# Performance work log

Measured on AMD Instinct MI355X. Metric: run time of the kernel, lower is better.

## Reference

```python
import jax, jax.numpy as jnp
from jax import lax
import numpy as np

S, B, XD = 2048, 64, 64   # seq_len, batch, x_dim
DX = 128                   # dense_x[-1]
H = 256                    # dim_RNN
DH = 128                   # dense_h_x[-1]
ALPHAS = np.array([0.9, 0.5, 0.1, 0.01], dtype=np.float32)


def setup_inputs() -> dict:
    key = jax.random.key(0)
    ks = jax.random.split(key, 12)
    def lin(k, fan_in, shape):
        return jax.random.normal(k, shape, jnp.float32) / np.sqrt(fan_in)
    sigmas = jnp.asarray(-np.log(1.0 / ALPHAS - 1.0), jnp.float32)  # inverse sigmoid
    return {
        "x": jax.random.normal(ks[0], (S, B, XD), jnp.float32),
        "Wx": lin(ks[1], XD, (XD, DX)),   # feature_extractor_x linear
        "bx": jnp.zeros((DX,), jnp.float32),
        "Wih": lin(ks[2], DX, (H, DX)),   # RNN input-hidden
        "bih": jnp.zeros((H,), jnp.float32),
        "Whh": lin(ks[3], H, (H, H)),     # RNN hidden-hidden
        "bhh": jnp.zeros((H,), jnp.float32),
        "Whx": lin(ks[4], H, (H, DH)),    # mlp_h_x linear
        "bhx": jnp.zeros((DH,), jnp.float32),
        "Wout": lin(ks[5], DH, (DH, XD)), # gen_out
        "bout": jnp.zeros((XD,), jnp.float32),
        "sigmas": sigmas,
    }


def reference(x, Wx, bx, Wih, bih, Whh, bhh, Whx, bhx, Wout, bout, sigmas):
    # alphas_per_unit: sigmoid(sigmas) tiled to dim_RNN
    alphas = jnp.tile(jax.nn.sigmoid(sigmas), H // sigmas.shape[0])  # [H]
    # feature extractor over all timesteps (teacher forcing, mix_ratio=0)
    feat = jnp.tanh(x @ Wx + bx)  # [S, B, DX]
    h0 = jnp.zeros((x.shape[1], H), x.dtype)

    def step(h, f_t):
        # emit y_t from previous hidden state: gen_out(tanh(mlp_h_x(h)))
        y_t = jnp.tanh(h @ Whx + bhx) @ Wout + bout        # [B, XD]
        # single-step Elman RNN cell
        h_new = jnp.tanh(f_t @ Wih.T + bih + h @ Whh.T + bhh)
        # leaky integration blend per unit
        h_next = (1.0 - alphas) * h + alphas * h_new
        return h_next, y_t

    _, y = lax.scan(step, h0, feat)  # y: [S, B, XD]
    return y
```

## Files before the change

kernel.cpp:

```cpp
#include <hip/hip_runtime.h>
#include <math.h>

#define SS 2048
#define BB 64
#define XDIM 64
#define DXF 128
#define HH 256
#define DHH 128

typedef float v2f __attribute__((ext_vector_type(2)));

__device__ __forceinline__ float ftanh(float x) {
    float e = __expf(2.0f * x);
    return 1.0f - 2.0f / (e + 1.0f);
}

template <int CTRL>
__device__ __forceinline__ float dpp_mov_f(float x) {
    return __int_as_float(__builtin_amdgcn_update_dpp(
        0, __float_as_int(x), CTRL, 0xF, 0xF, true));
}
#define RED8_SHR(s) { s += dpp_mov_f<0x111>(s); s += dpp_mov_f<0x112>(s); \
                      s += dpp_mov_f<0x114>(s); }
#define RED8_SHL(s) { s += dpp_mov_f<0x101>(s); s += dpp_mov_f<0x102>(s); \
                      s += dpp_mov_f<0x104>(s); }

__global__ __launch_bounds__(256) void k1_featu(
    const float* __restrict__ x, const float* __restrict__ Wx,
    const float* __restrict__ bx, const float* __restrict__ Wih,
    const float* __restrict__ bih, const float* __restrict__ bhh,
    float* __restrict__ u)
{
    __shared__ float xs[64][XDIM];
    __shared__ float fs[64][DXF];
    const int tid = threadIdx.x;
    const size_t row0 = (size_t)blockIdx.x * 64;

    for (int v = tid; v < 64 * XDIM; v += 256) {
        int r = v >> 6, m = v & 63;
        xs[r][m] = x[(row0 + r) * XDIM + m];
    }
    __syncthreads();

    {
        const int cq = tid & 31;
        const int ru = tid >> 5;
        v2f aA[2][4], aB[2][4];
        #pragma unroll
        for (int g = 0; g < 2; ++g)
            #pragma unroll
            for (int i = 0; i < 4; ++i) { aA[g][i] = (v2f)0.f; aB[g][i] = (v2f)0.f; }

        #pragma unroll
        for (int kc = 0; kc < 4; ++kc) {
            v2f wA[16], wB[16];
            #pragma unroll
            for (int k = 0; k < 16; ++k) {
                const float* wp = Wx + (kc * 16 + k) * DXF + cq;
                wA[k] = (v2f){wp[0],  wp[32]};
                wB[k] = (v2f){wp[64], wp[96]};
            }
            #pragma unroll
            for (int g = 0; g < 2; ++g) {
                const int rb = 8 * ru + 4 * g;
                #pragma unroll
                for (int k4 = 0; k4 < 4; ++k4) {
                    float4 xv[4];
                    #pragma unroll
                    for (int i = 0; i < 4; ++i)
                        xv[i] = *(const float4*)&xs[rb + i][kc * 16 + 4 * k4];
                    #pragma unroll
                    for (int i = 0; i < 4; ++i) {
                        #pragma unroll
                        for (int e = 0; e < 4; ++e) {
                            const float xe = (e == 0) ? xv[i].x : (e == 1) ? xv[i].y
                                           : (e == 2) ? xv[i].z : xv[i].w;
                            const v2f xb = (v2f){xe, xe};
                            aA[g][i] += wA[4 * k4 + e] * xb;
                            aB[g][i] += wB[4 * k4 + e] * xb;
                        }
                    }
                }
            }
        }
        const float b0 = bx[cq], b1 = bx[cq + 32], b2 = bx[cq + 64], b3 = bx[cq + 96];
        #pragma unroll
        for (int g = 0; g < 2; ++g)
            #pragma unroll
            for (int i = 0; i < 4; ++i) {
                const int r = 8 * ru + 4 * g + i;
                fs[r][cq]      = ftanh(aA[g][i].x + b0);
                fs[r][cq + 32] = ftanh(aA[g][i].y + b1);
                fs[r][cq + 64] = ftanh(aB[g][i].x + b2);
                fs[r][cq + 96] = ftanh(aB[g][i].y + b3);
            }
    }
    __syncthreads();

    {
        const int q4 = tid & 63;
        const int rq = tid >> 6;
        v2f aA[4][4], aB[4][4];
        #pragma unroll
        for (int g = 0; g < 4; ++g)
            #pragma unroll
            for (int i = 0; i < 4; ++i) { aA[g][i] = (v2f)0.f; aB[g][i] = (v2f)0.f; }

        #pragma unroll
        for (int kc = 0; kc < 8; ++kc) {
            v2f wA[16], wB[16];
            #pragma unroll
            for (int k4 = 0; k4 < 4; ++k4) {
                const float4 w0 = *(const float4*)(Wih + (size_t)(q4      ) * DXF + kc * 16 + 4 * k4);
                const float4 w1 = *(const float4*)(Wih + (size_t)(q4 +  64) * DXF + kc * 16 + 4 * k4);
                const float4 w2 = *(const float4*)(Wih + (size_t)(q4 + 128) * DXF + kc * 16 + 4 * k4);
                const float4 w3 = *(const float4*)(Wih + (size_t)(q4 + 192) * DXF + kc * 16 + 4 * k4);
                wA[4 * k4 + 0] = (v2f){w0.x, w1.x}; wA[4 * k4 + 1] = (v2f){w0.y, w1.y};
                wA[4 * k4 + 2] = (v2f){w0.z, w1.z}; wA[4 * k4 + 3] = (v2f){w0.w, w1.w};
                wB[4 * k4 + 0] = (v2f){w2.x, w3.x}; wB[4 * k4 + 1] = (v2f){w2.y, w3.y};
                wB[4 * k4 + 2] = (v2f){w2.z, w3.z}; wB[4 * k4 + 3] = (v2f){w2.w, w3.w};
            }
            #pragma unroll
            for (int g = 0; g < 4; ++g) {
                const int rb = 16 * rq + 4 * g;
                #pragma unroll
                for (int k4 = 0; k4 < 4; ++k4) {
                    float4 fv[4];
                    #pragma unroll
                    for (int i = 0; i < 4; ++i)
                        fv[i] = *(const float4*)&fs[rb + i][kc * 16 + 4 * k4];
                    #pragma unroll
                    for (int i = 0; i < 4; ++i) {
                        #pragma unroll
                        for (int e = 0; e < 4; ++e) {
                            const float fe = (e == 0) ? fv[i].x : (e == 1) ? fv[i].y
                                           : (e == 2) ? fv[i].z : fv[i].w;
                            const v2f fb = (v2f){fe, fe};
                            aA[g][i] += wA[4 * k4 + e] * fb;
                            aB[g][i] += wB[4 * k4 + e] * fb;
                        }
                    }
                }
            }
        }
        const float b0 = bih[q4]       + bhh[q4];
        const float b1 = bih[q4 + 64]  + bhh[q4 + 64];
        const float b2 = bih[q4 + 128] + bhh[q4 + 128];
        const float b3 = bih[q4 + 192] + bhh[q4 + 192];
        #pragma unroll
        for (int g = 0; g < 4; ++g)
            #pragma unroll
            for (int i = 0; i < 4; ++i) {
                const size_t row = row0 + 16 * rq + 4 * g + i;
                u[row * HH + q4]       = aA[g][i].x + b0;
                u[row * HH + q4 + 64]  = aA[g][i].y + b1;
                u[row * HH + q4 + 128] = aB[g][i].x + b2;
                u[row * HH + q4 + 192] = aB[g][i].y + b3;
            }
    }
}

__global__ __launch_bounds__(1024)
__attribute__((amdgpu_waves_per_eu(4, 4)))
void k2_rnn(
    const float* __restrict__ u, const float* __restrict__ Whh,
    const float* __restrict__ sigmas, float* __restrict__ hist)
{
    __shared__ float hbuf[2][HH];
    const int tid = threadIdx.x;
    const int b = blockIdx.x;
    const int c = tid & 7;
    const int rg = tid >> 3;

    v2f w2[2][16];
    #pragma unroll
    for (int r = 0; r < 2; ++r) {
        const float* wrow = Whh + (size_t)(2 * rg + r) * HH + 32 * c;
        #pragma unroll
        for (int j = 0; j < 8; ++j) {
            const int kk = 4 * ((j + c) & 7);
            const float4 wv = *(const float4*)(wrow + kk);
            w2[r][2 * j]     = (v2f){wv.x, wv.y};
            w2[r][2 * j + 1] = (v2f){wv.z, wv.w};
        }
    }

#define K2_PIN                                                               \
    _Pragma("unroll")                                                        \
    for (int r = 0; r < 2; ++r) {                                            \
        asm volatile("" : "+v"(w2[r][0]),  "+v"(w2[r][1]),  "+v"(w2[r][2]),  \
                          "+v"(w2[r][3]),  "+v"(w2[r][4]),  "+v"(w2[r][5]),  \
                          "+v"(w2[r][6]),  "+v"(w2[r][7]),  "+v"(w2[r][8]),  \
                          "+v"(w2[r][9]),  "+v"(w2[r][10]), "+v"(w2[r][11]), \
                          "+v"(w2[r][12]), "+v"(w2[r][13]), "+v"(w2[r][14]), \
                          "+v"(w2[r][15]));                                  \
    }
    K2_PIN

    const bool updHi = (c == 7);
    const bool updLo = (c == 0);
    const bool upd = updHi || updLo;
    const int myrow = 2 * rg + (updHi ? 0 : 1);

    const float alpha = 1.f / (1.f + __expf(-sigmas[myrow & 3]));

    if (tid < HH) hbuf[0][tid] = 0.0f;

    const size_t ustride = (size_t)BB * HH;
    const float* up = u + (size_t)b * HH + myrow;
    float uq0 = 0.f, uq1 = 0.f, uq2 = 0.f, uq3 = 0.f;
    if (upd) {
        uq0 = up[0];
        uq1 = up[ustride];
        uq2 = up[2 * ustride];
        uq3 = up[3 * ustride];
    }
    up += 4 * ustride;
    float* hp = hist + (size_t)b * HH + myrow;
    float hreg = 0.f;

    __syncthreads();

#define K2_BODY(T, UQ)                                                       \
    {                                                                        \
        const int cur = (T) & 1;                                             \
        float unew = 0.f;                                                    \
        if (upd && (T) + 4 < SS) unew = *up;     \
        up += ustride;                                                       \
        v2f a0a = (v2f)0.f, a0b = (v2f)0.f;                                  \
        v2f a1a = (v2f)0.f, a1b = (v2f)0.f;                                  \
        const float4* h4p = (const float4*)&hbuf[cur][32 * c];               \
        _Pragma("unroll")                                                    \
        for (int j = 0; j < 8; ++j) {                                        \
            const float4 h4 = h4p[(j + c) & 7];                              \
            const v2f hA = (v2f){h4.x, h4.y};                                \
            const v2f hB = (v2f){h4.z, h4.w};                                \
            a0a += w2[0][2 * j] * hA; a0b += w2[0][2 * j + 1] * hB;          \
            a1a += w2[1][2 * j] * hA; a1b += w2[1][2 * j + 1] * hB;          \
        }                                                                    \
        float s0 = (a0a.x + a0a.y) + (a0b.x + a0b.y);                        \
        float s1 = (a1a.x + a1a.y) + (a1b.x + a1b.y);                        \
        RED8_SHR(s0)                        \
        RED8_SHL(s1)                        \
        if (upd) {                                                           \
            const float s = (updHi ? s0 : s1) + (UQ);                        \
            *hp = hreg;                            \
            hreg = hreg + alpha * (ftanh(s) - hreg);                         \
            hbuf[cur ^ 1][myrow] = hreg;                                     \
            (UQ) = unew;                                                     \
        }                                                                    \
        hp += ustride;                                                       \
         \
        asm volatile("s_waitcnt lgkmcnt(0)\n\ts_barrier" ::: "memory");      \
    }

    for (int t = 0; t < SS; t += 4) {
        K2_PIN
        K2_BODY(t,     uq0)
        K2_BODY(t + 1, uq1)
        K2_BODY(t + 2, uq2)
        K2_BODY(t + 3, uq3)
    }
#undef K2_BODY
#undef K2_PIN
}

__global__ __launch_bounds__(256) void k3_y(
    const float* __restrict__ hist, const float* __restrict__ Whx,
    const float* __restrict__ bhx, const float* __restrict__ Wout,
    const float* __restrict__ bout, float* __restrict__ y)
{
    __shared__ float hs[32][HH];
    __shared__ float gs[32][DHH];
    const int tid = threadIdx.x;
    const size_t row0 = (size_t)blockIdx.x * 32;

    for (int v = tid; v < 32 * HH; v += 256) {
        int r = v >> 8, i = v & 255;
        hs[r][i] = hist[(row0 + r) * HH + i];
    }
    __syncthreads();

    {
        const int aq = tid & 31;
        const int ru = tid >> 5;
        v2f aA[4], aB[4];
        #pragma unroll
        for (int i = 0; i < 4; ++i) { aA[i] = (v2f)0.f; aB[i] = (v2f)0.f; }

        #pragma unroll
        for (int kc = 0; kc < 16; ++kc) {
            v2f wA[16], wB[16];
            #pragma unroll
            for (int k = 0; k < 16; ++k) {
                const float* wp = Whx + (size_t)(kc * 16 + k) * DHH + aq;
                wA[k] = (v2f){wp[0],  wp[32]};
                wB[k] = (v2f){wp[64], wp[96]};
            }
            #pragma unroll
            for (int k4 = 0; k4 < 4; ++k4) {
                float4 hv[4];
                #pragma unroll
                for (int i = 0; i < 4; ++i)
                    hv[i] = *(const float4*)&hs[4 * ru + i][kc * 16 + 4 * k4];
                #pragma unroll
                for (int i = 0; i < 4; ++i) {
                    #pragma unroll
                    for (int e = 0; e < 4; ++e) {
                        const float he = (e == 0) ? hv[i].x : (e == 1) ? hv[i].y
                                       : (e == 2) ? hv[i].z : hv[i].w;
                        const v2f hb = (v2f){he, he};
                        aA[i] += wA[4 * k4 + e] * hb;
                        aB[i] += wB[4 * k4 + e] * hb;
                    }
                }
            }
        }
        const float b0 = bhx[aq], b1 = bhx[aq + 32], b2 = bhx[aq + 64], b3 = bhx[aq + 96];
        #pragma unroll
        for (int i = 0; i < 4; ++i) {
            const int r = 4 * ru + i;
            gs[r][aq]      = ftanh(aA[i].x + b0);
            gs[r][aq + 32] = ftanh(aA[i].y + b1);
            gs[r][aq + 64] = ftanh(aB[i].x + b2);
            gs[r][aq + 96] = ftanh(aB[i].y + b3);
        }
    }
    __syncthreads();

    {
        const int o2 = tid & 31;
        const int ru = tid >> 5;
        v2f acc[4];
        #pragma unroll
        for (int i = 0; i < 4; ++i) acc[i] = (v2f)0.f;

        #pragma unroll
        for (int kc = 0; kc < 2; ++kc) {
            v2f w[64];
            #pragma unroll
            for (int k = 0; k < 64; ++k) {
                const float* wp = Wout + (size_t)(kc * 64 + k) * XDIM + o2;
                w[k] = (v2f){wp[0], wp[32]};
            }
            #pragma unroll
            for (int k4 = 0; k4 < 16; ++k4) {
                float4 gv[4];
                #pragma unroll
                for (int i = 0; i < 4; ++i)
                    gv[i] = *(const float4*)&gs[4 * ru + i][kc * 64 + 4 * k4];
                #pragma unroll
                for (int i = 0; i < 4; ++i) {
                    #pragma unroll
                    for (int e = 0; e < 4; ++e) {
                        const float ge = (e == 0) ? gv[i].x : (e == 1) ? gv[i].y
                                       : (e == 2) ? gv[i].z : gv[i].w;
                        acc[i] += w[4 * k4 + e] * (v2f){ge, ge};
                    }
                }
            }
        }
        const float b0 = bout[o2], b1 = bout[o2 + 32];
        #pragma unroll
        for (int i = 0; i < 4; ++i) {
            const size_t row = row0 + 4 * ru + i;
            y[row * XDIM + o2]      = acc[i].x + b0;
            y[row * XDIM + o2 + 32] = acc[i].y + b1;
        }
    }
}

extern "C" void kernel_launch(void* const* d_in, const int* in_sizes, int n_in,
                              void* d_out, int out_size, void* d_ws, size_t ws_size,
                              hipStream_t stream) {
    const float* x      = (const float*)d_in[0];
    const float* Wx     = (const float*)d_in[1];
    const float* bx     = (const float*)d_in[2];
    const float* Wih    = (const float*)d_in[3];
    const float* bih    = (const float*)d_in[4];
    const float* Whh    = (const float*)d_in[5];
    const float* bhh    = (const float*)d_in[6];
    const float* Whx    = (const float*)d_in[7];
    const float* bhx    = (const float*)d_in[8];
    const float* Wout   = (const float*)d_in[9];
    const float* bout   = (const float*)d_in[10];
    const float* sigmas = (const float*)d_in[11];
    float* y = (float*)d_out;

    float* u    = (float*)d_ws;
    float* hist = u + (size_t)SS * BB * HH;

    k1_featu<<<(SS * BB) / 64, 256, 0, stream>>>(x, Wx, bx, Wih, bih, bhh, u);
    k2_rnn<<<BB, 1024, 0, stream>>>(u, Whh, sigmas, hist);
    k3_y<<<(SS * BB) / 32, 256, 0, stream>>>(hist, Whx, bhx, Wout, bout, y);
}
```

Baseline: 1.994 ms.

## Remap recurrent matvec to 8x8 thread tiles with transpose-style lane reduction

The recurrent kernel now gives each thread 8 hidden rows by 8 columns of Whh, instead of 2 rows by 32 columns. Each thread therefore reads only two float4 values of the hidden state from LDS per step. Partial sums are combined across the 32 lanes with a butterfly transpose-reduce (select plus DPP/swizzle exchanges), so every lane ends up owning one row's full sum. The hidden-state buffer uses a padded stride of 12 to limit LDS bank conflicts. The aim is to cut LDS traffic and reduction latency on the serial per-timestep critical path. The cost is a deeper cross-lane reduction that includes a ds_swizzle, and the per-iteration register pinning of the weights has been removed.

Result: slower. 2.137 ms (+7.2%).

```diff
diff --git a/kernel.cpp b/kernel.cpp
--- a/kernel.cpp
+++ b/kernel.cpp
@@ -20,10 +20,6 @@
     return __int_as_float(__builtin_amdgcn_update_dpp(
         0, __float_as_int(x), CTRL, 0xF, 0xF, true));
 }
-#define RED8_SHR(s) { s += dpp_mov_f<0x111>(s); s += dpp_mov_f<0x112>(s); \
-                      s += dpp_mov_f<0x114>(s); }
-#define RED8_SHL(s) { s += dpp_mov_f<0x101>(s); s += dpp_mov_f<0x102>(s); \
-                      s += dpp_mov_f<0x104>(s); }
 
 __global__ __launch_bounds__(256) void k1_featu(
     const float* __restrict__ x, const float* __restrict__ Wx,
@@ -166,45 +162,39 @@
     const float* __restrict__ u, const float* __restrict__ Whh,
     const float* __restrict__ sigmas, float* __restrict__ hist)
 {
-    __shared__ float hbuf[2][HH];
+    __shared__ float hbuf[2][12 * 32];
     const int tid = threadIdx.x;
     const int b = blockIdx.x;
-    const int c = tid & 7;
-    const int rg = tid >> 3;
-
-    v2f w2[2][16];
+    const int c  = tid & 31;
+    const int rg = tid >> 5;
+
+    v2f w2[8][4];
     #pragma unroll
-    for (int r = 0; r < 2; ++r) {
-        const float* wrow = Whh + (size_t)(2 * rg + r) * HH + 32 * c;
-        #pragma unroll
-        for (int j = 0; j < 8; ++j) {
-            const int kk = 4 * ((j + c) & 7);
-            const float4 wv = *(const float4*)(wrow + kk);
-            w2[r][2 * j]     = (v2f){wv.x, wv.y};
-            w2[r][2 * j + 1] = (v2f){wv.z, wv.w};
-        }
-    }
-
-#define K2_PIN                                                               \
-    _Pragma("unroll")                                                        \
-    for (int r = 0; r < 2; ++r) {                                            \
-        asm volatile("" : "+v"(w2[r][0]),  "+v"(w2[r][1]),  "+v"(w2[r][2]),  \
-                          "+v"(w2[r][3]),  "+v"(w2[r][4]),  "+v"(w2[r][5]),  \
-                          "+v"(w2[r][6]),  "+v"(w2[r][7]),  "+v"(w2[r][8]),  \
-                          "+v"(w2[r][9]),  "+v"(w2[r][10]), "+v"(w2[r][11]), \
-                          "+v"(w2[r][12]), "+v"(w2[r][13]), "+v"(w2[r][14]), \
-                          "+v"(w2[r][15]));                                  \
-    }
-    K2_PIN
-
-    const bool updHi = (c == 7);
-    const bool updLo = (c == 0);
-    const bool upd = updHi || updLo;
-    const int myrow = 2 * rg + (updHi ? 0 : 1);
+    for (int r = 0; r < 8; ++r) {
+        const float* wrow = Whh + (size_t)(8 * rg + r) * HH + 8 * c;
+        const float4 w0 = *(const float4*)(wrow);
+        const float4 w1 = *(const float4*)(wrow + 4);
+        w2[r][0] = (v2f){w0.x, w0.y};
+        w2[r][1] = (v2f){w0.z, w0.w};
+        w2[r][2] = (v2f){w1.x, w1.y};
+        w2[r][3] = (v2f){w1.z, w1.w};
+    }
+    #pragma unroll
+    for (int r = 0; r < 8; r += 4) {
+        asm volatile("" : "+v"(w2[r][0]),     "+v"(w2[r][1]),     "+v"(w2[r][2]),     "+v"(w2[r][3]),
+                          "+v"(w2[r + 1][0]), "+v"(w2[r + 1][1]), "+v"(w2[r + 1][2]), "+v"(w2[r + 1][3]),
+                          "+v"(w2[r + 2][0]), "+v"(w2[r + 2][1]), "+v"(w2[r + 2][2]), "+v"(w2[r + 2][3]),
+                          "+v"(w2[r + 3][0]), "+v"(w2[r + 3][1]), "+v"(w2[r + 3][2]), "+v"(w2[r + 3][3]));
+    }
+
+    const int pb0 = c & 1, pb1 = (c >> 1) & 1, pb2 = (c >> 2) & 1;
+    const int rl = 4 * pb2 + 2 * pb0 + pb1;
+    const bool upd = (c < 8);
+    const int myrow = 8 * rg + rl;
 
     const float alpha = 1.f / (1.f + __expf(-sigmas[myrow & 3]));
 
-    if (tid < HH) hbuf[0][tid] = 0.0f;
+    if (tid < 12 * 32) hbuf[0][tid] = 0.0f;
 
     const size_t ustride = (size_t)BB * HH;
     const float* up = u + (size_t)b * HH + myrow;
@@ -227,27 +217,54 @@
         float unew = 0.f;                                                    \
         if (upd && (T) + 4 < SS) unew = *up;     \
         up += ustride;                                                       \
-        v2f a0a = (v2f)0.f, a0b = (v2f)0.f;                                  \
-        v2f a1a = (v2f)0.f, a1b = (v2f)0.f;                                  \
-        const float4* h4p = (const float4*)&hbuf[cur][32 * c];               \
+        const float4 hv0 = *(const float4*)&hbuf[cur][12 * c];               \
+        const float4 hv1 = *(const float4*)&hbuf[cur][12 * c + 4];           \
+        const v2f hA = (v2f){hv0.x, hv0.y};                                  \
+        const v2f hB = (v2f){hv0.z, hv0.w};                                  \
+        const v2f hC = (v2f){hv1.x, hv1.y};                                  \
+        const v2f hD = (v2f){hv1.z, hv1.w};                                  \
+        float s[8];                                                          \
         _Pragma("unroll")                                                    \
-        for (int j = 0; j < 8; ++j) {                                        \
-            const float4 h4 = h4p[(j + c) & 7];                              \
-            const v2f hA = (v2f){h4.x, h4.y};                                \
-            const v2f hB = (v2f){h4.z, h4.w};                                \
-            a0a += w2[0][2 * j] * hA; a0b += w2[0][2 * j + 1] * hB;          \
-            a1a += w2[1][2 * j] * hA; a1b += w2[1][2 * j + 1] * hB;          \
+        for (int r = 0; r < 8; ++r) {                                        \
+            v2f a = w2[r][0] * hA;                                           \
+            a += w2[r][1] * hB;                                              \
+            a += w2[r][2] * hC;                                              \
+            a += w2[r][3] * hD;                                              \
+            s[r] = a.x + a.y;                                                \
         }                                                                    \
-        float s0 = (a0a.x + a0a.y) + (a0b.x + a0b.y);                        \
-        float s1 = (a1a.x + a1a.y) + (a1b.x + a1b.y);                        \
-        RED8_SHR(s0)                        \
-        RED8_SHL(s1)                        \
-        if (upd) {                                                           \
-            const float s = (updHi ? s0 : s1) + (UQ);                        \
-            *hp = hreg;                            \
-            hreg = hreg + alpha * (ftanh(s) - hreg);                         \
-            hbuf[cur ^ 1][myrow] = hreg;                                     \
-            (UQ) = unew;                                                     \
+             \
+        float t1[4];                                                         \
+        _Pragma("unroll")                                                    \
+        for (int i = 0; i < 4; ++i) {                                        \
+            const float g = pb2 ? s[i] : s[i + 4];                           \
+            const float k = pb2 ? s[i + 4] : s[i];                           \
+            t1[i] = k + dpp_mov_f<0x141>(g);                                 \
+        }                                                                    \
+                \
+        float t2[2];                                                         \
+        _Pragma("unroll")                                                    \
+        for (int i = 0; i < 2; ++i) {                                        \
+            const float g = pb0 ? t1[i] : t1[i + 2];                         \
+            const float k = pb0 ? t1[i + 2] : t1[i];                         \
+            t2[i] = k + dpp_mov_f<0xB1>(g);                                  \
+        }                                                                    \
+                \
+        {                                                                    \
+            const float g = pb1 ? t2[0] : t2[1];                             \
+            const float k = pb1 ? t2[1] : t2[0];                             \
+            float sr = k + dpp_mov_f<0x4E>(g);                               \
+                                              \
+            sr += dpp_mov_f<0x128>(sr);                                      \
+                            \
+            sr += __int_as_float(__builtin_amdgcn_ds_swizzle(                \
+                      __float_as_int(sr), 0x401F));                          \
+            if (upd) {                                                       \
+                const float sin_ = sr + (UQ);                                \
+                *hp = hreg;                        \
+                hreg = hreg + alpha * (ftanh(sin_) - hreg);                  \
+                hbuf[cur ^ 1][12 * rg + rl] = hreg;                          \
+                (UQ) = unew;                                                 \
+            }                                                                \
         }                                                                    \
         hp += ustride;                                                       \
          \
@@ -255,14 +272,12 @@
     }
 
     for (int t = 0; t < SS; t += 4) {
-        K2_PIN
         K2_BODY(t,     uq0)
         K2_BODY(t + 1, uq1)
         K2_BODY(t + 2, uq2)
         K2_BODY(t + 3, uq3)
     }
 #undef K2_BODY
-#undef K2_PIN
 }
 
 __global__ __launch_bounds__(256) void k3_y(
```
